# Kernel tuning notes

Measured on AMD Instinct MI355X. Metric: run time of the kernel, lower is better.

The kernel has to match this reference:

```python
import jax, jax.numpy as jnp
import numpy as np

ANCHORS = np.array([[10.,13.],[16.,30.],[33.,23.],[30.,61.],[62.,45.],
                    [59.,119.],[116.,90.],[156.,198.],[373.,326.]], dtype=np.float32)
ANCHOR_MASK = [[6,7,8],[3,4,5],[0,1,2]]
INPUT_WH = np.array([320., 320.], dtype=np.float32)  # (W, H) == input_shape[::-1] (square)
IGNORE_THRESH = 0.5
NUM_CLASSES = 80
GRIDS = [10, 20, 40]
BATCH = 4


def _bce_logits(labels, logits):
    # tf.nn.sigmoid_cross_entropy_with_logits
    return jnp.maximum(logits, 0.0) - logits * labels + jnp.log1p(jnp.exp(-jnp.abs(logits)))


def _yolo_head(feats, anchors):
    gh, gw = feats.shape[1], feats.shape[2]
    gx = jnp.arange(gw, dtype=feats.dtype)
    gy = jnp.arange(gh, dtype=feats.dtype)
    # grid[..., 0] = x, grid[..., 1] = y ; shape [gh, gw, 1, 2]
    grid = jnp.stack(jnp.meshgrid(gx, gy), axis=-1)[:, :, None, :]
    box_xy = (jax.nn.sigmoid(feats[..., :2]) + grid) / jnp.array([gw, gh], feats.dtype)
    anc = jnp.asarray(anchors, feats.dtype).reshape(1, 1, 1, -1, 2)
    box_wh = jnp.exp(feats[..., 2:4]) * anc / jnp.asarray(INPUT_WH, feats.dtype)
    return grid, box_xy, box_wh


def _pairwise_iou(p, t):
    # p: [B,P,4] pred boxes (cx,cy,w,h); t: [B,N,4] true boxes -> iou [B,P,N]
    p_min = p[:, :, None, :2] - p[:, :, None, 2:4] * 0.5
    p_max = p[:, :, None, :2] + p[:, :, None, 2:4] * 0.5
    t_min = t[:, None, :, :2] - t[:, None, :, 2:4] * 0.5
    t_max = t[:, None, :, :2] + t[:, None, :, 2:4] * 0.5
    wh = jnp.maximum(jnp.minimum(p_max, t_max) - jnp.maximum(p_min, t_min), 0.0)
    inter = wh[..., 0] * wh[..., 1]
    p_area = p[:, :, None, 2] * p[:, :, None, 3]
    t_area = t[:, None, :, 2] * t[:, None, :, 3]
    return inter / (p_area + t_area - inter)


def _layer_loss(t, y, anchors, g):
    obj = t[..., 4:5]                      # [B,g,g,3,1]
    objb = obj != 0
    grid, pxy, pwh = _yolo_head(y, anchors)
    pred_box = jnp.concatenate([pxy, pwh], axis=-1)
    raw_true_xy = t[..., :2] * jnp.array([g, g], t.dtype) - grid
    anc = jnp.asarray(anchors, t.dtype).reshape(1, 1, 1, -1, 2)
    wh_scaled = t[..., 2:4] * jnp.asarray(INPUT_WH, t.dtype) / anc
    raw_true_wh = jnp.where(objb, jnp.log(jnp.where(objb, wh_scaled, 1.0)), 0.0)
    box_scale = 2.0 - t[..., 2:3] * t[..., 3:4]

    # ignore mask: masked pairwise IoU (all-slots, statically shaped; mask = objectness)
    B = t.shape[0]
    P = g * g * 3
    pb = pred_box.reshape(B, P, 4)
    tb = t[..., :4].reshape(B, P, 4)
    tmask = (t[..., 4] != 0).reshape(B, P)
    iou = _pairwise_iou(pb, tb)                         # [B,P,P]
    iou = jnp.where(tmask[:, None, :], iou, -jnp.inf)
    best_iou = jnp.max(iou, axis=-1)                    # -inf when no true boxes (matches empty reduce_max)
    ignore = (best_iou < IGNORE_THRESH).astype(t.dtype).reshape(obj.shape)

    xy_loss = obj * box_scale * _bce_logits(raw_true_xy, y[..., 0:2])
    wh_loss = obj * box_scale * 0.5 * jnp.square(raw_true_wh - y[..., 2:4])
    conf_loss = (obj + (1.0 - obj) * ignore) * _bce_logits(obj, y[..., 4:5])
    cls_loss = obj * _bce_logits(t[..., 5:], y[..., 5:])

    per_img = (xy_loss.sum((1, 2, 3, 4)) + wh_loss.sum((1, 2, 3, 4))
               + conf_loss.sum((1, 2, 3, 4)) + cls_loss.sum((1, 2, 3, 4)))
    return jnp.mean(per_img)


def setup_inputs() -> dict:
    key = jax.random.key(0)
    inp = {}
    for l, g in enumerate(GRIDS):
        k = jax.random.fold_in(key, l)
        k1, k2, k3, k4, k5 = jax.random.split(k, 5)
        xy = jax.random.uniform(k1, (BATCH, g, g, 3, 2), jnp.float32)
        wh = jax.random.uniform(k2, (BATCH, g, g, 3, 2), jnp.float32, 0.05, 0.9)
        obj = jax.random.bernoulli(k3, 0.02, (BATCH, g, g, 3, 1)).astype(jnp.float32)
        cls = jax.random.uniform(k4, (BATCH, g, g, 3, NUM_CLASSES), jnp.float32)
        inp[f"t{l}"] = jnp.concatenate([xy, wh, obj, cls], axis=-1)
        inp[f"y{l}"] = jax.random.normal(k5, (BATCH, g, g, 3, 5 + NUM_CLASSES), jnp.float32)
    return inp


def reference(t0, t1, t2, y0, y1, y2):
    targets = [t0, t1, t2]
    outputs = [y0, y1, y2]
    loss = jnp.float32(0.0)
    for l in range(3):
        loss = loss + _layer_loss(targets[l], outputs[l], ANCHORS[ANCHOR_MASK[l]], GRIDS[l])
    return loss
```

## Files before the change

kernel.cpp:

```cpp
#include <hip/hip_runtime.h>
#include <math.h>

#define NBLK 104
#define SCAP 512
#define CAP0 64
#define CAP1 128
#define CAP2 512

__device__ __constant__ float c_anc[3][3][2] = {
  {{116.f, 90.f}, {156.f, 198.f}, {373.f, 326.f}},
  {{ 30.f, 61.f}, { 62.f,  45.f}, { 59.f, 119.f}},
  {{ 10.f, 13.f}, { 16.f,  30.f}, { 33.f,  23.f}}};

__device__ __forceinline__ float bce_f(float label, float logit) {
    return fmaxf(logit, 0.0f) - logit * label + log1pf(expf(-fabsf(logit)));
}

__global__ void k_init(int* __restrict__ counts, int* __restrict__ done) {
    if (threadIdx.x < 16) counts[threadIdx.x] = 0;
    if (threadIdx.x == 16) *done = 0;
}

__global__ __launch_bounds__(256) void k_compact(
    const float* __restrict__ t0, const float* __restrict__ t1, const float* __restrict__ t2,
    int* __restrict__ counts, float4* __restrict__ boxes)
{
    int gid = blockIdx.x * 256 + threadIdx.x;
    if (gid >= 25200) return;
    const float* t; int l, idx, P, cap, base;
    if (gid < 1200)      { l = 0; idx = gid;        t = t0; P = 300;  cap = CAP0; base = 0;   }
    else if (gid < 6000) { l = 1; idx = gid - 1200; t = t1; P = 1200; cap = CAP1; base = 256; }
    else                 { l = 2; idx = gid - 6000; t = t2; P = 4800; cap = CAP2; base = 768; }
    const float* tp = t + (size_t)idx * 85;
    float obj = tp[4];
    if (obj != 0.0f) {
        int img = idx / P;
        int slotBase = base + img * cap;
        int s = atomicAdd(&counts[l * 4 + img], 1);
        if (s < cap) {
            float tx = tp[0], ty = tp[1], tw = tp[2], th = tp[3];
            boxes[slotBase + s] = make_float4(tx - tw * 0.5f, ty - th * 0.5f,
                                              tx + tw * 0.5f, ty + th * 0.5f);
        }
    }
}

template<int P, int G>
__device__ __forceinline__ float layer_block(
    const float* __restrict__ t, const float* __restrict__ y,
    int img, int chunk, int cap, int slotBase, const float (*anc)[2],
    const int* __restrict__ counts, const float4* __restrict__ boxes,
    float4* sbox, int lw)
{
    const int tid = threadIdx.x;
    const float* tslab = t + (size_t)img * P * 85;
    const float* yslab = y + (size_t)img * P * 85;

    int pos = chunk * 256 + tid;
    bool valid = pos < P;
    int ppre = valid ? pos : 0;
    const float* yp = yslab + (size_t)ppre * 85;
    float q0 = yp[0], q1 = yp[1], q2 = yp[2], q3 = yp[3], q4 = yp[4];
    float obj = tslab[(size_t)ppre * 85 + 4];
    if (!valid) obj = 0.0f;

    int cnt = counts[lw];
    if (cnt > cap) cnt = cap;
    int cntPad = (cnt + 7) & ~7;
    for (int k = tid; k < cntPad; k += 256)
        sbox[k] = (k < cnt) ? boxes[slotBase + k]
                            : make_float4(0.f, 0.f, 0.f, 0.f);
    __syncthreads();

    float acc = 0.0f;
    if (valid) {
        int a = pos % 3, cell = pos / 3;
        int j = cell % G, i = cell / G;
        float aw = anc[a][0], ah = anc[a][1];
        float gi = (float)G;

        float px = (1.0f / (1.0f + expf(-q0)) + (float)j) / gi;
        float py = (1.0f / (1.0f + expf(-q1)) + (float)i) / gi;
        float pw = expf(q2) * aw * (1.0f / 320.0f);
        float ph = expf(q3) * ah * (1.0f / 320.0f);
        float phx = pw * 0.5f, phy = ph * 0.5f;
        float pminx = px - phx, pmaxx = px + phx;
        float pminy = py - phy, pmaxy = py + phy;
        float pa = pw * ph;

        float m = -1.0f;
        for (int k0 = 0; k0 < cntPad; k0 += 8) {
            float mm[8];
            #pragma unroll
            for (int u = 0; u < 8; ++u) {
                float4 tb = sbox[k0 + u];
                float wx = fminf(pmaxx, tb.z) - fmaxf(pminx, tb.x);
                float wy = fminf(pmaxy, tb.w) - fmaxf(pminy, tb.y);
                wx = fmaxf(wx, 0.0f);
                wy = fmaxf(wy, 0.0f);
                float inter = wx * wy;
                float ta = (tb.z - tb.x) * (tb.w - tb.y);
                mm[u] = 3.0f * inter - pa - ta;
            }
            float a0 = fmaxf(mm[0], mm[1]), a1 = fmaxf(mm[2], mm[3]);
            float a2 = fmaxf(mm[4], mm[5]), a3 = fmaxf(mm[6], mm[7]);
            m = fmaxf(m, fmaxf(fmaxf(a0, a1), fmaxf(a2, a3)));
        }
        float ignore = (m < 0.0f) ? 1.0f : 0.0f;
        float bce_c = fmaxf(q4, 0.0f) - q4 * obj + log1pf(expf(-fabsf(q4)));
        acc = (obj + (1.0f - obj) * ignore) * bce_c;
    }

    unsigned long long mb = __ballot(valid && obj != 0.0f);
    int lane = tid & 63;
    int waveBase = chunk * 256 + (tid & ~63);
    while (mb) {
        int b = __ffsll(mb) - 1; mb &= mb - 1;
        int ppos = waveBase + b;
        const float* tp = tslab + (size_t)ppos * 85;
        const float* ypp = yslab + (size_t)ppos * 85;
        float tv1 = tp[lane], yv1 = ypp[lane];
        bool has2 = lane < 21;
        float tv2 = 0.f, yv2 = 0.f;
        if (has2) { tv2 = tp[lane + 64]; yv2 = ypp[lane + 64]; }

        float tw = __shfl(tv1, 2, 64);
        float th = __shfl(tv1, 3, 64);
        float bs = 2.0f - tw * th;
        int a = ppos % 3, cell = ppos / 3;
        int jj = cell % G, ii = cell / G;
        float aw = anc[a][0], ah = anc[a][1];

        float term;
        if (lane == 0)      term = bs * bce_f(tv1 * (float)G - (float)jj, yv1);
        else if (lane == 1) term = bs * bce_f(tv1 * (float)G - (float)ii, yv1);
        else if (lane == 2) { float d = logf(tv1 * 320.0f / aw) - yv1; term = bs * 0.5f * d * d; }
        else if (lane == 3) { float d = logf(tv1 * 320.0f / ah) - yv1; term = bs * 0.5f * d * d; }
        else if (lane == 4) term = 0.0f;
        else                term = bce_f(tv1, yv1);
        if (has2) term += bce_f(tv2, yv2);
        acc += term;
    }
    return acc;
}

__global__ __launch_bounds__(256) void k_main(
    const float* __restrict__ t0, const float* __restrict__ y0,
    const float* __restrict__ t1, const float* __restrict__ y1,
    const float* __restrict__ t2, const float* __restrict__ y2,
    const int* __restrict__ counts, const float4* __restrict__ boxes,
    float* __restrict__ partials, int* __restrict__ done,
    float* __restrict__ out)
{
    __shared__ float4 sbox[SCAP];
    int blk = blockIdx.x;

    float acc;
    if (blk < 8) {
        int img = blk >> 1;
        acc = layer_block< 300, 10>(t0, y0, img, blk & 1, CAP0, img * CAP0,
                                    c_anc[0], counts, boxes, sbox, img);
    } else if (blk < 28) {
        int r = blk - 8, img = r / 5;
        acc = layer_block<1200, 20>(t1, y1, img, r % 5, CAP1, 256 + img * CAP1,
                                    c_anc[1], counts, boxes, sbox, 4 + img);
    } else {
        int r = blk - 28, img = r / 19;
        acc = layer_block<4800, 40>(t2, y2, img, r % 19, CAP2, 768 + img * CAP2,
                                    c_anc[2], counts, boxes, sbox, 8 + img);
    }

    float v = acc;
    #pragma unroll
    for (int o = 32; o > 0; o >>= 1) v += __shfl_down(v, o, 64);
    __shared__ float red[4];
    int lane = threadIdx.x & 63, w = threadIdx.x >> 6;
    if (lane == 0) red[w] = v;
    __syncthreads();

    if (threadIdx.x < 64) {
        int old = 0;
        if (threadIdx.x == 0) {
            float p = ((red[0] + red[1]) + (red[2] + red[3])) * 0.25f;
            __hip_atomic_store(&partials[blk], p, __ATOMIC_RELAXED, __HIP_MEMORY_SCOPE_AGENT);
            old = __hip_atomic_fetch_add(done, 1, __ATOMIC_ACQ_REL, __HIP_MEMORY_SCOPE_AGENT);
        }
        old = __shfl(old, 0, 64);
        if (old == NBLK - 1) {
            float s = 0.0f;
            if (lane < NBLK - 64)
                s = __hip_atomic_load(&partials[lane + 64], __ATOMIC_RELAXED, __HIP_MEMORY_SCOPE_AGENT);
            s += __hip_atomic_load(&partials[lane], __ATOMIC_RELAXED, __HIP_MEMORY_SCOPE_AGENT);
            #pragma unroll
            for (int o = 32; o > 0; o >>= 1) s += __shfl_down(s, o, 64);
            if (lane == 0) out[0] = s;
        }
    }
}

extern "C" void kernel_launch(void* const* d_in, const int* in_sizes, int n_in,
                              void* d_out, int out_size, void* d_ws, size_t ws_size,
                              hipStream_t stream) {
    const float* t0 = (const float*)d_in[0];
    const float* y0 = (const float*)d_in[1];
    const float* t1 = (const float*)d_in[2];
    const float* y1 = (const float*)d_in[3];
    const float* t2 = (const float*)d_in[4];
    const float* y2 = (const float*)d_in[5];

    int*    counts   = (int*)d_ws;
    int*    done     = (int*)((char*)d_ws + 64);
    float4* boxes    = (float4*)((char*)d_ws + 128);
    float*  partials = (float*)((char*)d_ws + 45184);
    float*  out      = (float*)d_out;

    k_init<<<1, 64, 0, stream>>>(counts, done);
    k_compact<<<99, 256, 0, stream>>>(t0, t1, t2, counts, boxes);
    k_main<<<NBLK, 256, 0, stream>>>(t0, y0, t1, y1, t2, y2, counts, boxes,
                                     partials, done, out);
}
```

Before: 34.24 us.

## Fuse compaction into main kernel with a grid-wide barrier

Replaces the init, compaction and main kernels with one fused kernel. Each block compacts its own object boxes into a per-block sublist, then all blocks spin on a global progress counter before gathering their image's sublists into shared memory. The same counter also serves the final reduction, and a memset replaces the init kernel. This removes two launches and the global atomic contention, but it relies on all 104 blocks being co-resident and caps each block at 32 objects.

After: 33.30 us. 2.7% less time.

```diff
diff --git a/kernel.cpp b/kernel.cpp
--- a/kernel.cpp
+++ b/kernel.cpp
@@ -2,10 +2,8 @@
 #include <math.h>
 
 #define NBLK 104
-#define SCAP 512
-#define CAP0 64
-#define CAP1 128
-#define CAP2 512
+#define SUBCAP 32
+#define SCAP 640
 
 __device__ __constant__ float c_anc[3][3][2] = {
   {{116.f, 90.f}, {156.f, 198.f}, {373.f, 326.f}},
@@ -16,43 +14,21 @@
     return fmaxf(logit, 0.0f) - logit * label + log1pf(expf(-fabsf(logit)));
 }
 
-__global__ void k_init(int* __restrict__ counts, int* __restrict__ done) {
-    if (threadIdx.x < 16) counts[threadIdx.x] = 0;
-    if (threadIdx.x == 16) *done = 0;
-}
-
-__global__ __launch_bounds__(256) void k_compact(
-    const float* __restrict__ t0, const float* __restrict__ t1, const float* __restrict__ t2,
-    int* __restrict__ counts, float4* __restrict__ boxes)
+__global__ __launch_bounds__(256) void k_fused(
+    const float* __restrict__ t0, const float* __restrict__ y0,
+    const float* __restrict__ t1, const float* __restrict__ y1,
+    const float* __restrict__ t2, const float* __restrict__ y2,
+    int* __restrict__ prog, int* __restrict__ subcnt,
+    float4* __restrict__ sublist, float* __restrict__ partials,
+    float* __restrict__ out)
 {
-    int gid = blockIdx.x * 256 + threadIdx.x;
-    if (gid >= 25200) return;
-    const float* t; int l, idx, P, cap, base;
-    if (gid < 1200)      { l = 0; idx = gid;        t = t0; P = 300;  cap = CAP0; base = 0;   }
-    else if (gid < 6000) { l = 1; idx = gid - 1200; t = t1; P = 1200; cap = CAP1; base = 256; }
-    else                 { l = 2; idx = gid - 6000; t = t2; P = 4800; cap = CAP2; base = 768; }
-    const float* tp = t + (size_t)idx * 85;
-    float obj = tp[4];
-    if (obj != 0.0f) {
-        int img = idx / P;
-        int slotBase = base + img * cap;
-        int s = atomicAdd(&counts[l * 4 + img], 1);
-        if (s < cap) {
-            float tx = tp[0], ty = tp[1], tw = tp[2], th = tp[3];
-            boxes[slotBase + s] = make_float4(tx - tw * 0.5f, ty - th * 0.5f,
-                                              tx + tw * 0.5f, ty + th * 0.5f);
-        }
-    }
-}
-
-template<int P, int G>
-__device__ __forceinline__ float layer_block(
-    const float* __restrict__ t, const float* __restrict__ y,
-    int img, int chunk, int cap, int slotBase, const float (*anc)[2],
-    const int* __restrict__ counts, const float4* __restrict__ boxes,
-    float4* sbox, int lw)
-{
-    const int tid = threadIdx.x;
+    const int blk = blockIdx.x, tid = threadIdx.x;
+    int img, chunk, P, G, imgBlkBase, nchunks;
+    const float *t, *y; const float (*anc)[2];
+    if (blk < 8)       { img = blk >> 1;          chunk = blk & 1;  P = 300;  G = 10; t = t0; y = y0; anc = c_anc[0]; imgBlkBase = img * 2;      nchunks = 2;  }
+    else if (blk < 28) { int r = blk - 8;  img = r / 5;  chunk = r % 5;  P = 1200; G = 20; t = t1; y = y1; anc = c_anc[1]; imgBlkBase = 8 + img * 5;  nchunks = 5;  }
+    else               { int r = blk - 28; img = r / 19; chunk = r % 19; P = 4800; G = 40; t = t2; y = y2; anc = c_anc[2]; imgBlkBase = 28 + img * 19; nchunks = 19; }
+
     const float* tslab = t + (size_t)img * P * 85;
     const float* yslab = y + (size_t)img * P * 85;
 
@@ -64,12 +40,46 @@
     float obj = tslab[(size_t)ppre * 85 + 4];
     if (!valid) obj = 0.0f;
 
-    int cnt = counts[lw];
-    if (cnt > cap) cnt = cap;
-    int cntPad = (cnt + 7) & ~7;
-    for (int k = tid; k < cntPad; k += 256)
-        sbox[k] = (k < cnt) ? boxes[slotBase + k]
-                            : make_float4(0.f, 0.f, 0.f, 0.f);
+    __shared__ int scnt;
+    if (tid == 0) scnt = 0;
+    __syncthreads();
+    int myslot = -1;
+    if (valid && obj != 0.0f) myslot = atomicAdd(&scnt, 1);
+    if (myslot >= 0 && myslot < SUBCAP) {
+        const float* tp = tslab + (size_t)pos * 85;
+        float tx = tp[0], ty = tp[1], tw = tp[2], th = tp[3];
+        sublist[blk * SUBCAP + myslot] =
+            make_float4(tx - tw * 0.5f, ty - th * 0.5f, tx + tw * 0.5f, ty + th * 0.5f);
+    }
+    __syncthreads();
+    if (tid == 0) {
+        int c = scnt; if (c > SUBCAP) c = SUBCAP;
+        subcnt[blk] = c;
+        __hip_atomic_fetch_add(prog, 1, __ATOMIC_RELEASE, __HIP_MEMORY_SCOPE_AGENT);
+        while (__hip_atomic_load(prog, __ATOMIC_ACQUIRE, __HIP_MEMORY_SCOPE_AGENT) < NBLK)
+            __builtin_amdgcn_s_sleep(2);
+    }
+    __syncthreads();
+
+    __shared__ float4 sbox[SCAP];
+    __shared__ int scounts[19], sprefix[20];
+    if (tid < nchunks) scounts[tid] = subcnt[imgBlkBase + tid];
+    __syncthreads();
+    if (tid == 0) {
+        int a0 = 0;
+        for (int c = 0; c < nchunks; ++c) { sprefix[c] = a0; a0 += scounts[c]; }
+        sprefix[nchunks] = a0;
+    }
+    __syncthreads();
+    int total = sprefix[nchunks];
+    for (int tp_ = tid; tp_ < nchunks * SUBCAP; tp_ += 256) {
+        int c = tp_ >> 5, s = tp_ & 31;
+        if (s < scounts[c]) sbox[sprefix[c] + s] = sublist[(imgBlkBase + c) * SUBCAP + s];
+    }
+    __syncthreads();
+    int cntPad = (total + 7) & ~7;
+    for (int k = total + tid; k < cntPad; k += 256)
+        sbox[k] = make_float4(0.f, 0.f, 0.f, 0.f);
     __syncthreads();
 
     float acc = 0.0f;
@@ -141,52 +151,24 @@
         if (has2) term += bce_f(tv2, yv2);
         acc += term;
     }
-    return acc;
-}
-
-__global__ __launch_bounds__(256) void k_main(
-    const float* __restrict__ t0, const float* __restrict__ y0,
-    const float* __restrict__ t1, const float* __restrict__ y1,
-    const float* __restrict__ t2, const float* __restrict__ y2,
-    const int* __restrict__ counts, const float4* __restrict__ boxes,
-    float* __restrict__ partials, int* __restrict__ done,
-    float* __restrict__ out)
-{
-    __shared__ float4 sbox[SCAP];
-    int blk = blockIdx.x;
-
-    float acc;
-    if (blk < 8) {
-        int img = blk >> 1;
-        acc = layer_block< 300, 10>(t0, y0, img, blk & 1, CAP0, img * CAP0,
-                                    c_anc[0], counts, boxes, sbox, img);
-    } else if (blk < 28) {
-        int r = blk - 8, img = r / 5;
-        acc = layer_block<1200, 20>(t1, y1, img, r % 5, CAP1, 256 + img * CAP1,
-                                    c_anc[1], counts, boxes, sbox, 4 + img);
-    } else {
-        int r = blk - 28, img = r / 19;
-        acc = layer_block<4800, 40>(t2, y2, img, r % 19, CAP2, 768 + img * CAP2,
-                                    c_anc[2], counts, boxes, sbox, 8 + img);
-    }
 
     float v = acc;
     #pragma unroll
     for (int o = 32; o > 0; o >>= 1) v += __shfl_down(v, o, 64);
     __shared__ float red[4];
-    int lane = threadIdx.x & 63, w = threadIdx.x >> 6;
+    int w = tid >> 6;
     if (lane == 0) red[w] = v;
     __syncthreads();
 
-    if (threadIdx.x < 64) {
+    if (tid < 64) {
         int old = 0;
-        if (threadIdx.x == 0) {
+        if (tid == 0) {
             float p = ((red[0] + red[1]) + (red[2] + red[3])) * 0.25f;
             __hip_atomic_store(&partials[blk], p, __ATOMIC_RELAXED, __HIP_MEMORY_SCOPE_AGENT);
-            old = __hip_atomic_fetch_add(done, 1, __ATOMIC_ACQ_REL, __HIP_MEMORY_SCOPE_AGENT);
+            old = __hip_atomic_fetch_add(prog, 1, __ATOMIC_ACQ_REL, __HIP_MEMORY_SCOPE_AGENT);
         }
         old = __shfl(old, 0, 64);
-        if (old == NBLK - 1) {
+        if (old == 2 * NBLK - 1) {
             float s = 0.0f;
             if (lane < NBLK - 64)
                 s = __hip_atomic_load(&partials[lane + 64], __ATOMIC_RELAXED, __HIP_MEMORY_SCOPE_AGENT);
@@ -208,14 +190,13 @@
     const float* t2 = (const float*)d_in[4];
     const float* y2 = (const float*)d_in[5];
 
-    int*    counts   = (int*)d_ws;
-    int*    done     = (int*)((char*)d_ws + 64);
-    float4* boxes    = (float4*)((char*)d_ws + 128);
-    float*  partials = (float*)((char*)d_ws + 45184);
+    int*    prog     = (int*)d_ws;
+    int*    subcnt   = (int*)((char*)d_ws + 64);
+    float4* sublist  = (float4*)((char*)d_ws + 1024);
+    float*  partials = (float*)((char*)d_ws + 54272);
     float*  out      = (float*)d_out;
 
-    k_init<<<1, 64, 0, stream>>>(counts, done);
-    k_compact<<<99, 256, 0, stream>>>(t0, t1, t2, counts, boxes);
-    k_main<<<NBLK, 256, 0, stream>>>(t0, y0, t1, y1, t2, y2, counts, boxes,
-                                     partials, done, out);
+    hipMemsetAsync(prog, 0, sizeof(int), stream);
+    k_fused<<<NBLK, 256, 0, stream>>>(t0, y0, t1, y1, t2, y2,
+                                      prog, subcnt, sublist, partials, out);
 }
```
